# Kernel optimization log

Measured on AMD Instinct MI355X. Metric: run time of the kernel, lower is better.

The kernel has to match this reference:

```python
import jax, jax.numpy as jnp
import numpy as np

B, N, E, H = 8, 2000, 20, 128


def setup_inputs() -> dict:
    key = jax.random.key(0)
    ks = jax.random.split(key, 9)
    s = 1.0 / np.sqrt(H)
    return {
        "x": jax.random.normal(ks[0], (B, N, H), dtype=jnp.float32),
        "e": jax.random.normal(ks[1], (B, N * E, H), dtype=jnp.float32),
        "Wu": jax.random.uniform(ks[2], (H, H), jnp.float32, -s, s),
        "bu": jax.random.uniform(ks[3], (H,), jnp.float32, -s, s),
        "Wv": jax.random.uniform(ks[4], (H, H), jnp.float32, -s, s),
        "bv": jax.random.uniform(ks[5], (H,), jnp.float32, -s, s),
        "We": jax.random.uniform(ks[6], (H, H), jnp.float32, -s, s),
        "be": jax.random.uniform(ks[7], (H,), jnp.float32, -s, s),
        "edge_index": jax.random.randint(ks[8], (B, N * E), 0, N, dtype=jnp.int32),
        "n_edges": E,
    }


def reference(x, e, Wu, bu, Wv, bv, We, be, edge_index, n_edges):
    b, n, h = x.shape
    Ux = x @ Wu + bu                      # [B, N, H] node self-embedding
    Vx = x @ Wv + bv                      # [B, N, H] neighbor embedding
    Ve = e @ We + be                      # [B, N*E, H] edge embedding
    # softmax over the n_edges axis per (node, channel)
    Ve = jax.nn.softmax(Ve.reshape(b, n, n_edges, h), axis=2)
    # gather neighbor features along node axis via edge_index
    Vx_g = jnp.take_along_axis(Vx, edge_index[..., None], axis=1)  # [B, N*E, H]
    to = (Ve * Vx_g.reshape(b, n, n_edges, h)).sum(axis=2)          # [B, N, H]
    return Ux + to
```

## Files before the change

### kernel.cpp

```cpp
#include <hip/hip_runtime.h>

#define B_   8
#define NN   2000
#define EE   20
#define HH   128
#define BN   (B_*NN)
#define NE   (NN*EE)

typedef unsigned short ushort_t;
typedef __bf16 bf16x8 __attribute__((ext_vector_type(8)));
typedef float  f32x4  __attribute__((ext_vector_type(4)));
typedef float  f4     __attribute__((ext_vector_type(4)));
typedef unsigned short us8 __attribute__((ext_vector_type(8)));
typedef unsigned short us4 __attribute__((ext_vector_type(4)));

union FragU { us8 u; bf16x8 b; };
union Frag32 { unsigned int w[4]; us8 u; bf16x8 b; };

__device__ __forceinline__ float b2f(ushort_t v) {
    union { unsigned int i; float f; } c; c.i = ((unsigned int)v) << 16; return c.f;
}
__device__ __forceinline__ ushort_t f2b(float f) {
    union { float f; unsigned int i; } c; c.f = f;
    unsigned int r = (c.i + 0x7FFFu + ((c.i >> 16) & 1u)) >> 16;
    return (ushort_t)r;
}

__global__ __launch_bounds__(256) void k1_embed(
    const float* __restrict__ x,
    const float* __restrict__ Wu, const float* __restrict__ bu,
    const float* __restrict__ Wv, const float* __restrict__ bv,
    ushort_t* __restrict__ Uxb, ushort_t* __restrict__ Vxb)
{
    const int tid  = threadIdx.x;
    const int lane = tid & 63;
    const int wave = tid >> 6;
    const int wm = wave >> 1, wn = wave & 1;
    const int q  = lane >> 4, ln = lane & 15;
    const int m0 = blockIdx.x * 64;
    const int sel = blockIdx.y;
    const float* W    = sel ? Wv : Wu;
    const float* bias = sel ? bv : bu;
    ushort_t* dst = sel ? Vxb : Uxb;

    FragU af[2][4];
#pragma unroll
    for (int tm = 0; tm < 2; ++tm)
#pragma unroll
        for (int ki = 0; ki < 4; ++ki) {
            const float* p = x + (size_t)(m0 + wm * 32 + tm * 16 + ln) * HH + ki * 32 + q * 8;
            f4 lo = *(const f4*)(p);
            f4 hi = *(const f4*)(p + 4);
            us8 t;
#pragma unroll
            for (int r = 0; r < 4; ++r) { t[r] = f2b(lo[r]); t[r + 4] = f2b(hi[r]); }
            af[tm][ki].u = t;
        }

    FragU bf[4][4];
#pragma unroll
    for (int ki = 0; ki < 4; ++ki)
#pragma unroll
        for (int tn = 0; tn < 4; ++tn) {
            int n = wn * 64 + tn * 16 + ln;
            us8 t;
#pragma unroll
            for (int i = 0; i < 8; ++i) t[i] = f2b(W[(ki * 32 + q * 8 + i) * HH + n]);
            bf[ki][tn].u = t;
        }

    f32x4 acc[2][4];
#pragma unroll
    for (int tm = 0; tm < 2; ++tm)
#pragma unroll
        for (int tn = 0; tn < 4; ++tn) acc[tm][tn] = (f32x4){0.f, 0.f, 0.f, 0.f};

#pragma unroll
    for (int ki = 0; ki < 4; ++ki)
#pragma unroll
        for (int tm = 0; tm < 2; ++tm)
#pragma unroll
            for (int tn = 0; tn < 4; ++tn)
                acc[tm][tn] = __builtin_amdgcn_mfma_f32_16x16x32_bf16(
                    af[tm][ki].b, bf[ki][tn].b, acc[tm][tn], 0, 0, 0);

#pragma unroll
    for (int tn = 0; tn < 4; ++tn) {
        int col = wn * 64 + tn * 16 + ln;
        float bb = bias[col];
#pragma unroll
        for (int tm = 0; tm < 2; ++tm) {
            int rowb = m0 + wm * 32 + tm * 16 + q * 4;
#pragma unroll
            for (int r = 0; r < 4; ++r)
                dst[(size_t)(rowb + r) * HH + col] = f2b(acc[tm][tn][r] + bb);
        }
    }
}

#define CSTR 84
#define GPB  8

__global__ __launch_bounds__(256, 2) void k2_fused(
    const float* __restrict__ e, const float* __restrict__ We,
    const int* __restrict__ eidx,
    const ushort_t* __restrict__ Uxb, const ushort_t* __restrict__ Vxb,
    float* __restrict__ out)
{
    __shared__ __align__(16) unsigned char smem[2][40960];

    const int tid  = threadIdx.x;
    const int lane = tid & 63;
    const int wave = tid >> 6;
    const int q  = lane >> 4, ln = lane & 15;
    const int rl = lane >> 5;
    const int sl = lane & 31;

    const int g0 = blockIdx.x * GPB;

    auto stage = [&](int g, int buf) {
        const int gb = g / 500;
        const int gl = g - gb * 500;
        const size_t er0 = (size_t)gb * NE + (size_t)gl * 80;
#pragma unroll
        for (int i = 0; i < 10; ++i) {
            const int r0 = wave * 20 + 2 * i;
            const int r  = r0 + rl;
            const int ss = sl ^ (r & 7);
            const float* gp = e + (er0 + r) * (size_t)HH + (ss << 2);
            __builtin_amdgcn_global_load_lds(
                (const __attribute__((address_space(1))) void*)gp,
                (__attribute__((address_space(3))) void*)(&smem[buf][r0 * 512]),
                16, 0, 0);
        }
    };

    stage(g0, 0);

    FragU bfr[4][2];
#pragma unroll
    for (int ki = 0; ki < 4; ++ki)
#pragma unroll
        for (int tn = 0; tn < 2; ++tn) {
            int n = wave * 32 + tn * 16 + ln;
            us8 t;
#pragma unroll
            for (int i = 0; i < 8; ++i) t[i] = f2b(We[(ki * 32 + q * 8 + i) * HH + n]);
            bfr[ki][tn].u = t;
        }

    int cur = 0;
#pragma unroll 1
    for (int t = 0; t < GPB; ++t) {
        const int g  = g0 + t;
        const int gb = g / 500;
        const int gl = g - gb * 500;
        const int nl0 = gl * 4;
        const size_t erow0 = (size_t)gb * NE + (size_t)nl0 * EE;

        int ridx = 0;
        if (tid < 80) ridx = eidx[erow0 + tid];

        if (t + 1 < GPB) stage(g + 1, cur ^ 1);

        if (t == 0)             asm volatile("s_waitcnt vmcnt(10)" ::: "memory");
        else if (t + 1 < GPB)   asm volatile("s_waitcnt vmcnt(12)" ::: "memory");
        else                    asm volatile("s_waitcnt vmcnt(2)"  ::: "memory");
        __builtin_amdgcn_s_barrier();

        const float* As = (const float*)smem[cur];
        f32x4 acc[5][2];
#pragma unroll
        for (int tm = 0; tm < 5; ++tm)
#pragma unroll
            for (int tn = 0; tn < 2; ++tn) acc[tm][tn] = (f32x4){0.f, 0.f, 0.f, 0.f};

#pragma unroll
        for (int ki = 0; ki < 4; ++ki) {
            Frag32 af[5];
#pragma unroll
            for (int tm = 0; tm < 5; ++tm) {
                const int r  = tm * 16 + ln;
                const int sw = r & 7;
                const int s0 = ki * 8 + q * 2;
                f4 lo = *(const f4*)(As + r * 128 + ((s0    ) ^ sw) * 4);
                f4 hi = *(const f4*)(As + r * 128 + ((s0 + 1) ^ sw) * 4);
                asm("v_cvt_pk_bf16_f32 %0, %1, %2" : "=v"(af[tm].w[0]) : "v"(lo[0]), "v"(lo[1]));
                asm("v_cvt_pk_bf16_f32 %0, %1, %2" : "=v"(af[tm].w[1]) : "v"(lo[2]), "v"(lo[3]));
                asm("v_cvt_pk_bf16_f32 %0, %1, %2" : "=v"(af[tm].w[2]) : "v"(hi[0]), "v"(hi[1]));
                asm("v_cvt_pk_bf16_f32 %0, %1, %2" : "=v"(af[tm].w[3]) : "v"(hi[2]), "v"(hi[3]));
            }
#pragma unroll
            for (int tm = 0; tm < 5; ++tm)
#pragma unroll
                for (int tn = 0; tn < 2; ++tn)
                    acc[tm][tn] = __builtin_amdgcn_mfma_f32_16x16x32_bf16(
                        af[tm].b, bfr[ki][tn].b, acc[tm][tn], 0, 0, 0);
        }

        __builtin_amdgcn_s_barrier();

        ushort_t* CT   = (ushort_t*)smem[cur];
        int*      sidx = (int*)(&smem[cur][38400]);
        if (tid < 80) sidx[tid] = ridx;
#pragma unroll
        for (int tm = 0; tm < 5; ++tm)
#pragma unroll
            for (int tn = 0; tn < 2; ++tn) {
                int col  = wave * 32 + tn * 16 + ln;
                int rowb = tm * 16 + q * 4;
                us4 pk;
#pragma unroll
                for (int r = 0; r < 4; ++r) pk[r] = f2b(acc[tm][tn][r]);
                *(us4*)(&CT[col * CSTR + rowb]) = pk;
            }

        asm volatile("s_waitcnt lgkmcnt(0)" ::: "memory");
        __builtin_amdgcn_s_barrier();

        const int h  = tid & 127;
        const int gp = tid >> 7;
#pragma unroll 1
        for (int j = 0; j < 2; ++j) {
            int gg = gp + 2 * j;
            const ushort_t* ctp = &CT[h * CSTR + gg * 20];
            float lv[20];
#pragma unroll
            for (int i = 0; i < 5; ++i) {
                us4 v = *(const us4*)(ctp + i * 4);
#pragma unroll
                for (int r = 0; r < 4; ++r) lv[i * 4 + r] = b2f(v[r]);
            }
            float mx = lv[0];
#pragma unroll
            for (int k = 1; k < EE; ++k) mx = fmaxf(mx, lv[k]);

            ushort_t gv[20];
            const int ib = gg * 20;
#pragma unroll
            for (int k = 0; k < EE; ++k)
                gv[k] = Vxb[(size_t)(gb * NN + sidx[ib + k]) * HH + h];

            float s = 0.f, a = 0.f;
#pragma unroll
            for (int k = 0; k < EE; ++k) {
                float p = __expf(lv[k] - mx);
                s += p;
                a = fmaf(p, b2f(gv[k]), a);
            }
            size_t orow = (size_t)(gb * NN + nl0 + gg) * HH + h;
            out[orow] = b2f(Uxb[orow]) + a / s;
        }

        __builtin_amdgcn_s_barrier();
        cur ^= 1;
    }
}

extern "C" void kernel_launch(void* const* d_in, const int* in_sizes, int n_in,
                              void* d_out, int out_size, void* d_ws, size_t ws_size,
                              hipStream_t stream) {
    const float* x  = (const float*)d_in[0];
    const float* e  = (const float*)d_in[1];
    const float* Wu = (const float*)d_in[2];
    const float* bu = (const float*)d_in[3];
    const float* Wv = (const float*)d_in[4];
    const float* bv = (const float*)d_in[5];
    const float* We = (const float*)d_in[6];
    const int*   eidx = (const int*)d_in[8];

    ushort_t* Uxb = (ushort_t*)d_ws;
    ushort_t* Vxb = (ushort_t*)((char*)d_ws + (size_t)BN * HH * 2);
    float*    o   = (float*)d_out;

    k1_embed<<<dim3(250, 2), 256, 0, stream>>>(x, Wu, bu, Wv, bv, Uxb, Vxb);
    k2_fused<<<dim3(500), 256, 0, stream>>>(e, We, eidx, Uxb, Vxb, o);
}
```

Before: 268.1 us.

## Prefetch gather indices and neighbor features before MFMA, drop softmax max pass

```diff
diff --git a/kernel.cpp b/kernel.cpp
--- a/kernel.cpp
+++ b/kernel.cpp
@@ -13,6 +13,7 @@
 typedef float  f4     __attribute__((ext_vector_type(4)));
 typedef unsigned short us8 __attribute__((ext_vector_type(8)));
 typedef unsigned short us4 __attribute__((ext_vector_type(4)));
+typedef int    i4     __attribute__((ext_vector_type(4)));
 
 union FragU { us8 u; bf16x8 b; };
 union Frag32 { unsigned int w[4]; us8 u; bf16x8 b; };
@@ -101,6 +102,10 @@
 #define CSTR 84
 #define GPB  8
 
+__device__ __forceinline__ void memfence_compiler() {
+    asm volatile("" ::: "memory");
+}
+
 __global__ __launch_bounds__(256, 2) void k2_fused(
     const float* __restrict__ e, const float* __restrict__ We,
     const int* __restrict__ eidx,
@@ -115,6 +120,8 @@
     const int q  = lane >> 4, ln = lane & 15;
     const int rl = lane >> 5;
     const int sl = lane & 31;
+    const int h  = tid & 127;
+    const int gp = tid >> 7;
 
     const int g0 = blockIdx.x * GPB;
 
@@ -127,9 +134,9 @@
             const int r0 = wave * 20 + 2 * i;
             const int r  = r0 + rl;
             const int ss = sl ^ (r & 7);
-            const float* gp = e + (er0 + r) * (size_t)HH + (ss << 2);
+            const float* gp_ = e + (er0 + r) * (size_t)HH + (ss << 2);
             __builtin_amdgcn_global_load_lds(
-                (const __attribute__((address_space(1))) void*)gp,
+                (const __attribute__((address_space(1))) void*)gp_,
                 (__attribute__((address_space(3))) void*)(&smem[buf][r0 * 512]),
                 16, 0, 0);
         }
@@ -145,7 +152,8 @@
             int n = wave * 32 + tn * 16 + ln;
             us8 t;
 #pragma unroll
-            for (int i = 0; i < 8; ++i) t[i] = f2b(We[(ki * 32 + q * 8 + i) * HH + n]);
+            for (int i = 0; i < 8; ++i)
+                t[i] = f2b(We[(ki * 32 + q * 8 + i) * HH + n] * 1.44269504089f);
             bfr[ki][tn].u = t;
         }
 
@@ -158,15 +166,37 @@
         const int nl0 = gl * 4;
         const size_t erow0 = (size_t)gb * NE + (size_t)nl0 * EE;
 
-        int ridx = 0;
-        if (tid < 80) ridx = eidx[erow0 + tid];
+        if (t == 0) asm volatile("s_waitcnt vmcnt(0)" ::: "memory");
+        else        asm volatile("s_waitcnt vmcnt(2)" ::: "memory");
+        memfence_compiler();
+        __builtin_amdgcn_s_barrier();
+        memfence_compiler();
+
+        i4 iv[2][5];
+#pragma unroll
+        for (int j = 0; j < 2; ++j) {
+            const int* ep = eidx + erow0 + (gp + 2 * j) * 20;
+#pragma unroll
+            for (int i = 0; i < 5; ++i) iv[j][i] = *(const i4*)(ep + i * 4);
+        }
+        ushort_t gv[2][20];
+        ushort_t uxv[2];
+        {
+            const ushort_t* vbase = Vxb + (size_t)gb * NN * HH + h;
+#pragma unroll
+            for (int j = 0; j < 2; ++j) {
+#pragma unroll
+                for (int i = 0; i < 5; ++i)
+#pragma unroll
+                    for (int r = 0; r < 4; ++r)
+                        gv[j][i * 4 + r] = vbase[(size_t)iv[j][i][r] * HH];
+                uxv[j] = Uxb[(size_t)(gb * NN + nl0 + gp + 2 * j) * HH + h];
+            }
+        }
+        __builtin_amdgcn_sched_barrier(0);
 
         if (t + 1 < GPB) stage(g + 1, cur ^ 1);
-
-        if (t == 0)             asm volatile("s_waitcnt vmcnt(10)" ::: "memory");
-        else if (t + 1 < GPB)   asm volatile("s_waitcnt vmcnt(12)" ::: "memory");
-        else                    asm volatile("s_waitcnt vmcnt(2)"  ::: "memory");
-        __builtin_amdgcn_s_barrier();
+        __builtin_amdgcn_sched_barrier(0);
 
         const float* As = (const float*)smem[cur];
         f32x4 acc[5][2];
@@ -198,11 +228,11 @@
                         af[tm].b, bfr[ki][tn].b, acc[tm][tn], 0, 0, 0);
         }
 
+        memfence_compiler();
         __builtin_amdgcn_s_barrier();
-
-        ushort_t* CT   = (ushort_t*)smem[cur];
-        int*      sidx = (int*)(&smem[cur][38400]);
-        if (tid < 80) sidx[tid] = ridx;
+        memfence_compiler();
+
+        ushort_t* CT = (ushort_t*)smem[cur];
 #pragma unroll
         for (int tm = 0; tm < 5; ++tm)
 #pragma unroll
@@ -217,42 +247,26 @@
 
         asm volatile("s_waitcnt lgkmcnt(0)" ::: "memory");
         __builtin_amdgcn_s_barrier();
-
-        const int h  = tid & 127;
-        const int gp = tid >> 7;
-#pragma unroll 1
+        memfence_compiler();
+
+#pragma unroll
         for (int j = 0; j < 2; ++j) {
-            int gg = gp + 2 * j;
+            const int gg = gp + 2 * j;
             const ushort_t* ctp = &CT[h * CSTR + gg * 20];
-            float lv[20];
+            float a = 0.f, s = 0.f;
 #pragma unroll
             for (int i = 0; i < 5; ++i) {
                 us4 v = *(const us4*)(ctp + i * 4);
 #pragma unroll
-                for (int r = 0; r < 4; ++r) lv[i * 4 + r] = b2f(v[r]);
-            }
-            float mx = lv[0];
-#pragma unroll
-            for (int k = 1; k < EE; ++k) mx = fmaxf(mx, lv[k]);
-
-            ushort_t gv[20];
-            const int ib = gg * 20;
-#pragma unroll
-            for (int k = 0; k < EE; ++k)
-                gv[k] = Vxb[(size_t)(gb * NN + sidx[ib + k]) * HH + h];
-
-            float s = 0.f, a = 0.f;
-#pragma unroll
-            for (int k = 0; k < EE; ++k) {
-                float p = __expf(lv[k] - mx);
-                s += p;
-                a = fmaf(p, b2f(gv[k]), a);
+                for (int r = 0; r < 4; ++r) {
+                    float p = exp2f(b2f(v[r]));
+                    s += p;
+                    a = fmaf(p, b2f(gv[j][i * 4 + r]), a);
+                }
             }
             size_t orow = (size_t)(gb * NN + nl0 + gg) * HH + h;
-            out[orow] = b2f(Uxb[orow]) + a / s;
-        }
-
-        __builtin_amdgcn_s_barrier();
+            out[orow] = b2f(uxv[j]) + a * __builtin_amdgcn_rcpf(s);
+        }
         cur ^= 1;
     }
 }
```

New measurement: 270.0 us. Within noise of the previous version (+0.7%).
